# Performance work log

Measured on AMD Instinct MI355X. Metric: run time of the kernel, lower is better.

Reference implementation:

```python
import jax, jax.numpy as jnp
import numpy as np
import math

D = 512          # belief_dim
H = 128          # hidden_dim
R = 64           # relation_dim
M = 8192         # max_beliefs
N = 131072       # candidate pairs
INIT_BIAS = math.log(0.4 / 0.6) * -1.0  # = log(1.5) ~ 0.405465


def _linear_params(key, fan_in, fan_out):
    kw, kb = jax.random.split(key)
    bound = 1.0 / math.sqrt(fan_in)
    W = jax.random.uniform(kw, (fan_in, fan_out), minval=-bound, maxval=bound, dtype=jnp.float32)
    b = jax.random.uniform(kb, (fan_out,), minval=-bound, maxval=bound, dtype=jnp.float32)
    return W, b


def setup_inputs() -> dict:
    key = jax.random.key(0)
    ks = jax.random.split(key, 11)
    beliefs = jax.random.normal(ks[0], (M, D), dtype=jnp.float32)
    src_idx = jax.random.randint(ks[1], (N,), 0, M)
    tgt_idx = jax.random.randint(ks[2], (N,), 0, M)
    # proposal_net: 3D -> H -> H//2 -> 1  (last bias = log(1.5))
    pw1, pb1 = _linear_params(ks[3], 3 * D, H)
    pw2, pb2 = _linear_params(ks[4], H, H // 2)
    pw3, _ = _linear_params(ks[5], H // 2, 1)
    pb3 = jnp.full((1,), INIT_BIAS, dtype=jnp.float32)
    # direction_net: 3D -> H//2 -> 1 (sigmoid)
    dw1, db1 = _linear_params(ks[6], 3 * D, H // 2)
    dw2, db2 = _linear_params(ks[7], H // 2, 1)
    # relation_net: 3D -> H -> R
    rw1, rb1 = _linear_params(ks[8], 3 * D, H)
    rw2, rb2 = _linear_params(ks[9], H, R)
    return {
        "beliefs": beliefs, "src_idx": src_idx, "tgt_idx": tgt_idx,
        "pw1": pw1, "pb1": pb1, "pw2": pw2, "pb2": pb2, "pw3": pw3, "pb3": pb3,
        "dw1": dw1, "db1": db1, "dw2": dw2, "db2": db2,
        "rw1": rw1, "rb1": rb1, "rw2": rw2, "rb2": rb2,
    }


def reference(beliefs, src_idx, tgt_idx,
              pw1, pb1, pw2, pb2, pw3, pb3,
              dw1, db1, dw2, db2,
              rw1, rb1, rw2, rb2):
    src = beliefs[src_idx]                       # [N, D] gather
    tgt = beliefs[tgt_idx]                       # [N, D] gather
    feats = jnp.concatenate([src, tgt, jnp.abs(src - tgt)], axis=-1)  # [N, 3D]

    # proposal head -> edge probability
    h = jax.nn.relu(feats @ pw1 + pb1)
    h = jax.nn.relu(h @ pw2 + pb2)
    probs = jax.nn.sigmoid((h @ pw3 + pb3)[:, 0])                     # [N]

    # direction head -> angle in [0, pi/2]
    d = jax.nn.relu(feats @ dw1 + db1)
    directions = jax.nn.sigmoid((d @ dw2 + db2)[:, 0]) * (jnp.pi / 2)  # [N]

    # relation head -> initial relation vectors
    r = jax.nn.relu(feats @ rw1 + rb1)
    relations = r @ rw2 + rb2                                          # [N, R]

    return probs, directions, relations
```

## Files before the change

kernel.cpp:

```cpp
#include <hip/hip_runtime.h>
#include <hip/hip_bf16.h>


#define DD 512
#define K3 1536
#define ROWS 128
#define LDACT 328
#define LDH 72

typedef short bf16x8 __attribute__((ext_vector_type(8)));
typedef float f32x4 __attribute__((ext_vector_type(4)));

__device__ inline float b2f(short s) {
    union { float f; unsigned u; } v;
    v.u = ((unsigned)(unsigned short)s) << 16;
    return v.f;
}
__device__ inline short f2b(float f) {
    union { float fl; unsigned u; } v;
    v.fl = f;
    unsigned x = v.u;
    unsigned r = x + 0x7fffu + ((x >> 16) & 1u);
    return (short)(r >> 16);
}
__device__ inline short babsdiff(short a, short b) {
    union { float f; unsigned u; } v;
    v.f = b2f(a) - b2f(b);
    return (short)((v.u & 0x7fffffffu) >> 16);
}

__device__ __forceinline__ int sidx(int seg, int kk2, int rt, int lane) {
    return (((seg * 2 + kk2) * 8 + rt) * 64 + lane) * 8;
}

#define WT_ELEMS (320 * 1536)
#define P2T_OFF WT_ELEMS
#define R2T_OFF (WT_ELEMS + 64 * 128)
#define PREP_TOT (WT_ELEMS + 2 * 64 * 128)
#define BEL_ELEMS (8192 * 512)
#define BEL_OFF PREP_TOT

__global__ void prep_kernel(const float* __restrict__ pw1,
                            const float* __restrict__ dw1,
                            const float* __restrict__ rw1,
                            const float* __restrict__ pw2,
                            const float* __restrict__ rw2,
                            const float* __restrict__ beliefs,
                            short* __restrict__ ws, int total) {
    int i = blockIdx.x * 256 + threadIdx.x;
    if (i >= total) return;
    if (i < WT_ELEMS) {
        int n = i / K3, k = i - n * K3;
        float v;
        if (n < 128)      v = pw1[k * 128 + n];
        else if (n < 192) v = dw1[k * 64 + (n - 128)];
        else              v = rw1[k * 128 + (n - 192)];
        ws[i] = f2b(v);
    } else if (i < R2T_OFF) {
        int j = i - P2T_OFF;
        int n = j >> 7, k = j & 127;
        ws[i] = f2b(pw2[k * 64 + n]);
    } else if (i < PREP_TOT) {
        int j = i - R2T_OFF;
        int n = j >> 7, k = j & 127;
        ws[i] = f2b(rw2[k * 64 + n]);
    } else {
        ws[i] = f2b(beliefs[i - BEL_OFF]);
    }
}

template<bool BF>
__global__ __launch_bounds__(256, 2) void edge_main(
    const float* __restrict__ beliefs, const short* __restrict__ bel16,
    const int* __restrict__ src_idx, const int* __restrict__ tgt_idx,
    const float* __restrict__ pb1, const float* __restrict__ db1,
    const float* __restrict__ rb1,
    const float* __restrict__ pb2, const float* __restrict__ pw3,
    const float* __restrict__ pb3,
    const float* __restrict__ dw2, const float* __restrict__ db2,
    const float* __restrict__ rb2,
    const short* __restrict__ WT, const short* __restrict__ pw2T,
    const short* __restrict__ rw2T,
    float* __restrict__ out, int N)
{
    __shared__ __align__(16) char smem_u[49152];
    __shared__ __align__(16) short h2s[64][LDH];
    __shared__ int sIdx[ROWS], tIdx[ROWS];

    short* As2 = (short*)smem_u;
    short (*acts)[LDACT] = (short (*)[LDACT])smem_u;

    const int t = threadIdx.x;
    const int r0 = blockIdx.x * ROWS;
    const int w = t >> 6, lane = t & 63, q = lane >> 4, ln = lane & 15;

    if (t < ROWS) sIdx[t] = src_idx[r0 + t] * DD;
    else tIdx[t - ROWS] = tgt_idx[r0 + t - ROWS] * DD;
    __syncthreads();

    f32x4 acc[5][8];
#pragma unroll
    for (int ct = 0; ct < 5; ct++)
#pragma unroll
        for (int rt = 0; rt < 8; rt++) acc[ct][rt] = (f32x4)(0.f);

    const int rrow = t >> 1, kk2w = t & 1;
    const int rtw = rrow >> 4, lnw = rrow & 15;
    const int cb32 = kk2w * 32;
    const int srow = sIdx[rrow], trow = tIdx[rrow];

    for (int k0 = 0; k0 < DD; k0 += 64) {
        if constexpr (BF) {
            const bf16x8* ps_ = (const bf16x8*)(bel16 + srow + k0 + cb32);
            const bf16x8* pt_ = (const bf16x8*)(bel16 + trow + k0 + cb32);
#pragma unroll
            for (int c = 0; c < 4; c++) {
                bf16x8 s8 = ps_[c], t8 = pt_[c], pa;
#pragma unroll
                for (int j = 0; j < 8; j++) pa[j] = babsdiff(s8[j], t8[j]);
                int l16 = c * 16 + lnw;
                *(bf16x8*)&As2[sidx(0, kk2w, rtw, l16)] = s8;
                *(bf16x8*)&As2[sidx(1, kk2w, rtw, l16)] = t8;
                *(bf16x8*)&As2[sidx(2, kk2w, rtw, l16)] = pa;
            }
        } else {
            const float4* ps_ = (const float4*)(beliefs + srow + k0 + cb32);
            const float4* pt_ = (const float4*)(beliefs + trow + k0 + cb32);
#pragma unroll
            for (int c = 0; c < 4; c++) {
                bf16x8 sb, tb, ab;
#pragma unroll
                for (int h = 0; h < 2; h++) {
                    float4 s4 = ps_[c * 2 + h], t4 = pt_[c * 2 + h];
                    float ss[4] = {s4.x, s4.y, s4.z, s4.w};
                    float tt[4] = {t4.x, t4.y, t4.z, t4.w};
#pragma unroll
                    for (int e = 0; e < 4; e++) {
                        int j = h * 4 + e;
                        sb[j] = f2b(ss[e]);
                        tb[j] = f2b(tt[e]);
                        ab[j] = f2b(fabsf(ss[e] - tt[e]));
                    }
                }
                int l16 = c * 16 + lnw;
                *(bf16x8*)&As2[sidx(0, kk2w, rtw, l16)] = sb;
                *(bf16x8*)&As2[sidx(1, kk2w, rtw, l16)] = tb;
                *(bf16x8*)&As2[sidx(2, kk2w, rtw, l16)] = ab;
            }
        }
        __syncthreads();

#pragma unroll
        for (int kk2 = 0; kk2 < 2; kk2++) {
#pragma unroll
            for (int seg = 0; seg < 3; seg++) {
                bf16x8 bfr[5];
#pragma unroll
                for (int ct = 0; ct < 5; ct++) {
                    int col = w * 80 + ct * 16 + ln;
                    bfr[ct] = *(const bf16x8*)(WT + (size_t)col * K3 +
                                               seg * DD + k0 + kk2 * 32 + q * 8);
                }
#pragma unroll
                for (int rt = 0; rt < 8; rt++) {
                    bf16x8 af = *(const bf16x8*)&As2[sidx(seg, kk2, rt, lane)];
#pragma unroll
                    for (int ct = 0; ct < 5; ct++)
                        acc[ct][rt] = __builtin_amdgcn_mfma_f32_16x16x32_bf16(
                            af, bfr[ct], acc[ct][rt], 0, 0, 0);
                }
            }
        }
        __syncthreads();
    }

#pragma unroll
    for (int h = 0; h < 2; h++) {
#pragma unroll
        for (int ct = 0; ct < 5; ct++) {
            int col = w * 80 + ct * 16 + ln;
            float bias = (col < 128) ? pb1[col]
                       : (col < 192) ? db1[col - 128]
                                     : rb1[col - 192];
#pragma unroll
            for (int rt4 = 0; rt4 < 4; rt4++)
#pragma unroll
                for (int i = 0; i < 4; i++) {
                    int lrow = rt4 * 16 + q * 4 + i;
                    float v = acc[ct][h * 4 + rt4][i] + bias;
                    acts[lrow][col] = f2b(fmaxf(v, 0.f));
                }
        }
        __syncthreads();

        {
            f32x4 rc[4];
#pragma unroll
            for (int rt = 0; rt < 4; rt++) rc[rt] = (f32x4)(0.f);
#pragma unroll
            for (int ks = 0; ks < 4; ks++) {
                bf16x8 bfr = *(const bf16x8*)(rw2T + (w * 16 + ln) * 128 +
                                              ks * 32 + q * 8);
#pragma unroll
                for (int rt = 0; rt < 4; rt++) {
                    bf16x8 afr = *(const bf16x8*)&acts[rt * 16 + ln][192 + ks * 32 + q * 8];
                    rc[rt] = __builtin_amdgcn_mfma_f32_16x16x32_bf16(afr, bfr, rc[rt], 0, 0, 0);
                }
            }
            int col = w * 16 + ln;
            float bias = rb2[col];
            float* rel = out + 2 * (size_t)N;
#pragma unroll
            for (int rt = 0; rt < 4; rt++)
#pragma unroll
                for (int i = 0; i < 4; i++) {
                    int grow = r0 + h * 64 + rt * 16 + q * 4 + i;
                    rel[(size_t)grow * 64 + col] = rc[rt][i] + bias;
                }
        }

        {
            f32x4 pc[4];
#pragma unroll
            for (int rt = 0; rt < 4; rt++) pc[rt] = (f32x4)(0.f);
#pragma unroll
            for (int ks = 0; ks < 4; ks++) {
                bf16x8 bfr = *(const bf16x8*)(pw2T + (w * 16 + ln) * 128 +
                                              ks * 32 + q * 8);
#pragma unroll
                for (int rt = 0; rt < 4; rt++) {
                    bf16x8 afr = *(const bf16x8*)&acts[rt * 16 + ln][0 + ks * 32 + q * 8];
                    pc[rt] = __builtin_amdgcn_mfma_f32_16x16x32_bf16(afr, bfr, pc[rt], 0, 0, 0);
                }
            }
            int col = w * 16 + ln;
            float bias = pb2[col];
#pragma unroll
            for (int rt = 0; rt < 4; rt++)
#pragma unroll
                for (int i = 0; i < 4; i++) {
                    int lrow = rt * 16 + q * 4 + i;
                    h2s[lrow][col] = f2b(fmaxf(pc[rt][i] + bias, 0.f));
                }
        }
        __syncthreads();

        if (t < 64) {
            float s = pb3[0];
#pragma unroll 8
            for (int k = 0; k < 64; k++) s += b2f(h2s[t][k]) * pw3[k];
            float pr = 1.f / (1.f + __expf(-s));
            out[r0 + h * 64 + t] = pr;
        } else if (t < 128) {
            int lrow = t - 64;
            float s = db2[0];
#pragma unroll 8
            for (int k = 0; k < 64; k++) s += b2f(acts[lrow][128 + k]) * dw2[k];
            float dir = (1.f / (1.f + __expf(-s))) * 1.57079632679489662f;
            out[(size_t)N + r0 + h * 64 + lrow] = dir;
        }
        __syncthreads();
    }
}

extern "C" void kernel_launch(void* const* d_in, const int* in_sizes, int n_in,
                              void* d_out, int out_size, void* d_ws, size_t ws_size,
                              hipStream_t stream) {
    const float* beliefs = (const float*)d_in[0];
    const int* src = (const int*)d_in[1];
    const int* tgt = (const int*)d_in[2];
    const float* pw1 = (const float*)d_in[3];
    const float* pb1 = (const float*)d_in[4];
    const float* pw2 = (const float*)d_in[5];
    const float* pb2 = (const float*)d_in[6];
    const float* pw3 = (const float*)d_in[7];
    const float* pb3 = (const float*)d_in[8];
    const float* dw1 = (const float*)d_in[9];
    const float* db1 = (const float*)d_in[10];
    const float* dw2 = (const float*)d_in[11];
    const float* db2 = (const float*)d_in[12];
    const float* rw1 = (const float*)d_in[13];
    const float* rb1 = (const float*)d_in[14];
    const float* rw2 = (const float*)d_in[15];
    const float* rb2 = (const float*)d_in[16];

    short* ws = (short*)d_ws;
    short* WT    = ws;
    short* pw2T  = ws + P2T_OFF;
    short* rw2T  = ws + R2T_OFF;
    short* bel16 = ws + BEL_OFF;
    const int N = in_sizes[1];

    const bool useBf = ws_size >= (size_t)(PREP_TOT + BEL_ELEMS) * sizeof(short);
    const int prepElems = useBf ? (PREP_TOT + BEL_ELEMS) : PREP_TOT;

    prep_kernel<<<(prepElems + 255) / 256, 256, 0, stream>>>(
        pw1, dw1, rw1, pw2, rw2, beliefs, ws, prepElems);

    if (useBf)
        edge_main<true><<<N / ROWS, 256, 0, stream>>>(
            beliefs, bel16, src, tgt, pb1, db1, rb1, pb2, pw3, pb3,
            dw2, db2, rb2, WT, pw2T, rw2T, (float*)d_out, N);
    else
        edge_main<false><<<N / ROWS, 256, 0, stream>>>(
            beliefs, bel16, src, tgt, pb1, db1, rb1, pb2, pw3, pb3,
            dw2, db2, rb2, WT, pw2T, rw2T, (float*)d_out, N);
}
```

Measured before the change: 277.8 us.

## Load gathered rows directly into MFMA A-fragments and tile weight transpose

Result: slower. 689.5 us (+148.2%).

```diff
diff --git a/kernel.cpp b/kernel.cpp
--- a/kernel.cpp
+++ b/kernel.cpp
@@ -29,10 +29,6 @@
     return (short)((v.u & 0x7fffffffu) >> 16);
 }
 
-__device__ __forceinline__ int sidx(int seg, int kk2, int rt, int lane) {
-    return (((seg * 2 + kk2) * 8 + rt) * 64 + lane) * 8;
-}
-
 #define WT_ELEMS (320 * 1536)
 #define P2T_OFF WT_ELEMS
 #define R2T_OFF (WT_ELEMS + 64 * 128)
@@ -40,32 +36,50 @@
 #define BEL_ELEMS (8192 * 512)
 #define BEL_OFF PREP_TOT
 
+#define TRANS_BLOCKS 480
+#define ELEM_TOT (2 * 64 * 128 + BEL_ELEMS)
+
 __global__ void prep_kernel(const float* __restrict__ pw1,
                             const float* __restrict__ dw1,
                             const float* __restrict__ rw1,
                             const float* __restrict__ pw2,
                             const float* __restrict__ rw2,
                             const float* __restrict__ beliefs,
-                            short* __restrict__ ws, int total) {
-    int i = blockIdx.x * 256 + threadIdx.x;
-    if (i >= total) return;
-    if (i < WT_ELEMS) {
-        int n = i / K3, k = i - n * K3;
-        float v;
-        if (n < 128)      v = pw1[k * 128 + n];
-        else if (n < 192) v = dw1[k * 64 + (n - 128)];
-        else              v = rw1[k * 128 + (n - 192)];
-        ws[i] = f2b(v);
-    } else if (i < R2T_OFF) {
-        int j = i - P2T_OFF;
-        int n = j >> 7, k = j & 127;
-        ws[i] = f2b(pw2[k * 64 + n]);
-    } else if (i < PREP_TOT) {
-        int j = i - R2T_OFF;
-        int n = j >> 7, k = j & 127;
-        ws[i] = f2b(rw2[k * 64 + n]);
+                            short* __restrict__ ws) {
+    const int bx = blockIdx.x, t = threadIdx.x;
+    if (bx < TRANS_BLOCKS) {
+        __shared__ short tile[32][33];
+        const int tk = (bx / 10) * 32, tn = (bx % 10) * 32;
+        const int r = t >> 5, c = t & 31;
+#pragma unroll
+        for (int p = 0; p < 4; p++) {
+            int k = tk + r + p * 8, n = tn + c;
+            float v;
+            if (n < 128)      v = pw1[k * 128 + n];
+            else if (n < 192) v = dw1[k * 64 + (n - 128)];
+            else              v = rw1[k * 128 + (n - 192)];
+            tile[r + p * 8][c] = f2b(v);
+        }
+        __syncthreads();
+#pragma unroll
+        for (int p = 0; p < 4; p++) {
+            int nn = tn + r + p * 8, kk = tk + c;
+            ws[(size_t)nn * K3 + kk] = tile[c][r + p * 8];
+        }
     } else {
-        ws[i] = f2b(beliefs[i - BEL_OFF]);
+        int j = (bx - TRANS_BLOCKS) * 256 + t;
+        if (j >= ELEM_TOT) return;
+        if (j < 8192) {
+            int n = j >> 7, k = j & 127;
+            ws[P2T_OFF + j] = f2b(pw2[k * 64 + n]);
+        } else if (j < 16384) {
+            int jj = j - 8192;
+            int n = jj >> 7, k = jj & 127;
+            ws[R2T_OFF + jj] = f2b(rw2[k * 64 + n]);
+        } else {
+            int idx = j - 16384;
+            ws[BEL_OFF + idx] = f2b(beliefs[idx]);
+        }
     }
 }
 
@@ -83,20 +97,20 @@
     const short* __restrict__ rw2T,
     float* __restrict__ out, int N)
 {
-    __shared__ __align__(16) char smem_u[49152];
-    __shared__ __align__(16) short h2s[64][LDH];
-    __shared__ int sIdx[ROWS], tIdx[ROWS];
-
-    short* As2 = (short*)smem_u;
-    short (*acts)[LDACT] = (short (*)[LDACT])smem_u;
+    __shared__ __align__(16) short smem[25600];
+    short (*acts)[LDACT] = (short (*)[LDACT])smem;
+    short (*h2s)[LDH] = (short (*)[LDH])(smem + 64 * LDACT);
 
     const int t = threadIdx.x;
     const int r0 = blockIdx.x * ROWS;
     const int w = t >> 6, lane = t & 63, q = lane >> 4, ln = lane & 15;
 
-    if (t < ROWS) sIdx[t] = src_idx[r0 + t] * DD;
-    else tIdx[t - ROWS] = tgt_idx[r0 + t - ROWS] * DD;
-    __syncthreads();
+    int offS[8], offT[8];
+#pragma unroll
+    for (int rt = 0; rt < 8; rt++) {
+        offS[rt] = src_idx[r0 + rt * 16 + ln] * DD;
+        offT[rt] = tgt_idx[r0 + rt * 16 + ln] * DD;
+    }
 
     f32x4 acc[5][8];
 #pragma unroll
@@ -104,78 +118,71 @@
 #pragma unroll
         for (int rt = 0; rt < 8; rt++) acc[ct][rt] = (f32x4)(0.f);
 
-    const int rrow = t >> 1, kk2w = t & 1;
-    const int rtw = rrow >> 4, lnw = rrow & 15;
-    const int cb32 = kk2w * 32;
-    const int srow = sIdx[rrow], trow = tIdx[rrow];
-
-    for (int k0 = 0; k0 < DD; k0 += 64) {
-        if constexpr (BF) {
-            const bf16x8* ps_ = (const bf16x8*)(bel16 + srow + k0 + cb32);
-            const bf16x8* pt_ = (const bf16x8*)(bel16 + trow + k0 + cb32);
-#pragma unroll
-            for (int c = 0; c < 4; c++) {
-                bf16x8 s8 = ps_[c], t8 = pt_[c], pa;
-#pragma unroll
-                for (int j = 0; j < 8; j++) pa[j] = babsdiff(s8[j], t8[j]);
-                int l16 = c * 16 + lnw;
-                *(bf16x8*)&As2[sidx(0, kk2w, rtw, l16)] = s8;
-                *(bf16x8*)&As2[sidx(1, kk2w, rtw, l16)] = t8;
-                *(bf16x8*)&As2[sidx(2, kk2w, rtw, l16)] = pa;
+    const int colbase = w * 80 + ln;
+    const int kq = q * 8;
+
+    for (int kc = 0; kc < DD; kc += 32) {
+        bf16x8 bS[5], bT[5], bA[5];
+#pragma unroll
+        for (int ct = 0; ct < 5; ct++) {
+            const short* base = WT + (size_t)(colbase + ct * 16) * K3 + kc + kq;
+            bS[ct] = *(const bf16x8*)(base);
+            bT[ct] = *(const bf16x8*)(base + DD);
+            bA[ct] = *(const bf16x8*)(base + 2 * DD);
+        }
+#pragma unroll
+        for (int half = 0; half < 2; half++) {
+            bf16x8 sF[4], tF[4];
+            if constexpr (BF) {
+#pragma unroll
+                for (int r4 = 0; r4 < 4; r4++) {
+                    sF[r4] = *(const bf16x8*)(bel16 + offS[half * 4 + r4] + kc + kq);
+                    tF[r4] = *(const bf16x8*)(bel16 + offT[half * 4 + r4] + kc + kq);
+                }
+            } else {
+#pragma unroll
+                for (int r4 = 0; r4 < 4; r4++) {
+                    const float* sp = beliefs + offS[half * 4 + r4] + kc + kq;
+                    const float* tp = beliefs + offT[half * 4 + r4] + kc + kq;
+                    float4 sa = *(const float4*)sp, sb = *(const float4*)(sp + 4);
+                    float4 ta = *(const float4*)tp, tb = *(const float4*)(tp + 4);
+                    float sv[8] = {sa.x, sa.y, sa.z, sa.w, sb.x, sb.y, sb.z, sb.w};
+                    float tv[8] = {ta.x, ta.y, ta.z, ta.w, tb.x, tb.y, tb.z, tb.w};
+#pragma unroll
+                    for (int j = 0; j < 8; j++) {
+                        sF[r4][j] = f2b(sv[j]);
+                        tF[r4][j] = f2b(tv[j]);
+                    }
+                }
             }
-        } else {
-            const float4* ps_ = (const float4*)(beliefs + srow + k0 + cb32);
-            const float4* pt_ = (const float4*)(beliefs + trow + k0 + cb32);
-#pragma unroll
-            for (int c = 0; c < 4; c++) {
-                bf16x8 sb, tb, ab;
-#pragma unroll
-                for (int h = 0; h < 2; h++) {
-                    float4 s4 = ps_[c * 2 + h], t4 = pt_[c * 2 + h];
-                    float ss[4] = {s4.x, s4.y, s4.z, s4.w};
-                    float tt[4] = {t4.x, t4.y, t4.z, t4.w};
-#pragma unroll
-                    for (int e = 0; e < 4; e++) {
-                        int j = h * 4 + e;
-                        sb[j] = f2b(ss[e]);
-                        tb[j] = f2b(tt[e]);
-                        ab[j] = f2b(fabsf(ss[e] - tt[e]));
-                    }
-                }
-                int l16 = c * 16 + lnw;
-                *(bf16x8*)&As2[sidx(0, kk2w, rtw, l16)] = sb;
-                *(bf16x8*)&As2[sidx(1, kk2w, rtw, l16)] = tb;
-                *(bf16x8*)&As2[sidx(2, kk2w, rtw, l16)] = ab;
+#pragma unroll
+            for (int r4 = 0; r4 < 4; r4++)
+#pragma unroll
+                for (int ct = 0; ct < 5; ct++)
+                    acc[ct][half * 4 + r4] = __builtin_amdgcn_mfma_f32_16x16x32_bf16(
+                        sF[r4], bS[ct], acc[ct][half * 4 + r4], 0, 0, 0);
+#pragma unroll
+            for (int r4 = 0; r4 < 4; r4++)
+#pragma unroll
+                for (int ct = 0; ct < 5; ct++)
+                    acc[ct][half * 4 + r4] = __builtin_amdgcn_mfma_f32_16x16x32_bf16(
+                        tF[r4], bT[ct], acc[ct][half * 4 + r4], 0, 0, 0);
+#pragma unroll
+            for (int r4 = 0; r4 < 4; r4++) {
+                bf16x8 aF;
+#pragma unroll
+                for (int j = 0; j < 8; j++) aF[j] = babsdiff(sF[r4][j], tF[r4][j]);
+#pragma unroll
+                for (int ct = 0; ct < 5; ct++)
+                    acc[ct][half * 4 + r4] = __builtin_amdgcn_mfma_f32_16x16x32_bf16(
+                        aF, bA[ct], acc[ct][half * 4 + r4], 0, 0, 0);
             }
         }
-        __syncthreads();
-
-#pragma unroll
-        for (int kk2 = 0; kk2 < 2; kk2++) {
-#pragma unroll
-            for (int seg = 0; seg < 3; seg++) {
-                bf16x8 bfr[5];
-#pragma unroll
-                for (int ct = 0; ct < 5; ct++) {
-                    int col = w * 80 + ct * 16 + ln;
-                    bfr[ct] = *(const bf16x8*)(WT + (size_t)col * K3 +
-                                               seg * DD + k0 + kk2 * 32 + q * 8);
-                }
-#pragma unroll
-                for (int rt = 0; rt < 8; rt++) {
-                    bf16x8 af = *(const bf16x8*)&As2[sidx(seg, kk2, rt, lane)];
-#pragma unroll
-                    for (int ct = 0; ct < 5; ct++)
-                        acc[ct][rt] = __builtin_amdgcn_mfma_f32_16x16x32_bf16(
-                            af, bfr[ct], acc[ct][rt], 0, 0, 0);
-                }
-            }
-        }
-        __syncthreads();
     }
 
 #pragma unroll
     for (int h = 0; h < 2; h++) {
+        if (h == 1) __syncthreads();
 #pragma unroll
         for (int ct = 0; ct < 5; ct++) {
             int col = w * 80 + ct * 16 + ln;
@@ -259,7 +266,6 @@
             float dir = (1.f / (1.f + __expf(-s))) * 1.57079632679489662f;
             out[(size_t)N + r0 + h * 64 + lrow] = dir;
         }
-        __syncthreads();
     }
 }
 
@@ -292,10 +298,11 @@
     const int N = in_sizes[1];
 
     const bool useBf = ws_size >= (size_t)(PREP_TOT + BEL_ELEMS) * sizeof(short);
-    const int prepElems = useBf ? (PREP_TOT + BEL_ELEMS) : PREP_TOT;
-
-    prep_kernel<<<(prepElems + 255) / 256, 256, 0, stream>>>(
-        pw1, dw1, rw1, pw2, rw2, beliefs, ws, prepElems);
+    const int elemN = useBf ? ELEM_TOT : (2 * 64 * 128);
+    const int prepBlocks = TRANS_BLOCKS + (elemN + 255) / 256;
+
+    prep_kernel<<<prepBlocks, 256, 0, stream>>>(pw1, dw1, rw1, pw2, rw2,
+                                                beliefs, ws);
 
     if (useBf)
         edge_main<true><<<N / ROWS, 256, 0, stream>>>(
```
